# Performance work log

Measured on AMD Instinct MI355X. Metric: run time of the kernel, lower is better.

## Reference

```python
import jax, jax.numpy as jnp
import numpy as np

N_NODES = 10000
N_EDGES = 320000
D = 128
H = 4
C = 128
L = 2
NEG_SLOPE = 0.2
LN_EPS = 1e-5


def setup_inputs() -> dict:
    key = jax.random.key(0)
    ks = jax.random.split(key, 8)
    x = jax.random.normal(ks[0], (N_NODES, D), dtype=jnp.float32)
    edge_index = jax.random.randint(ks[1], (2, N_EDGES), 0, N_NODES, dtype=jnp.int64)
    # weights scaled ~Glorot to keep attention logits in a sane range
    Wl = jax.random.normal(ks[2], (L, D, H * C), dtype=jnp.float32) * 0.1
    Wr = jax.random.normal(ks[3], (L, D, H * C), dtype=jnp.float32) * 0.1
    att = jax.random.normal(ks[4], (L, H, C), dtype=jnp.float32) * 0.1
    return {
        "x": x,
        "edge_index": edge_index,
        "Wl": Wl,
        "bl": jnp.zeros((L, H * C), jnp.float32),
        "Wr": Wr,
        "br": jnp.zeros((L, H * C), jnp.float32),
        "att": att,
        "bias": jnp.zeros((L, D), jnp.float32),
        "ln_g": jnp.ones((L, D), jnp.float32),
        "ln_b": jnp.zeros((L, D), jnp.float32),
    }


def _gatv2_layer(x, src, dst, Wl, bl, Wr, br, att, b):
    """GATv2Conv (concat=False -> head mean), messages src->dst, softmax over dst."""
    n = x.shape[0]
    xl = (x @ Wl + bl).reshape(n, H, C)  # source transform
    xr = (x @ Wr + br).reshape(n, H, C)  # target transform
    s = jax.nn.leaky_relu(xl[src] + xr[dst], NEG_SLOPE)  # [E, H, C]
    e = jnp.einsum("ehc,hc->eh", s, att)  # attention logits [E, H]
    m = jax.ops.segment_max(e, dst, num_segments=n)  # stable softmax per dst segment
    ex = jnp.exp(e - m[dst])
    denom = jax.ops.segment_sum(ex, dst, num_segments=n)
    alpha = ex / denom[dst]  # [E, H]
    out = jax.ops.segment_sum(alpha[:, :, None] * xl[src], dst, num_segments=n)  # [N, H, C]
    return out.mean(axis=1) + b  # concat=False -> mean over heads, then bias


def _layer_norm(h, g, b):
    mu = h.mean(-1, keepdims=True)
    var = ((h - mu) ** 2).mean(-1, keepdims=True)
    return (h - mu) * jax.lax.rsqrt(var + LN_EPS) * g + b


def reference(x, edge_index, Wl, bl, Wr, br, att, bias, ln_g, ln_b):
    n = x.shape[0]
    loop = jnp.arange(n, dtype=edge_index.dtype)
    src = jnp.concatenate([edge_index[0], loop])  # add self-loops (PyG default)
    dst = jnp.concatenate([edge_index[1], loop])
    for i in range(L):
        h = _gatv2_layer(x, src, dst, Wl[i], bl[i], Wr[i], br[i], att[i], bias[i])
        x = h + x  # residual
        x = jax.nn.relu(_layer_norm(x, ln_g[i], ln_b[i]))
    return x
```

## Files before the change

kernel.cpp:

```cpp
#include <hip/hip_runtime.h>
#include <math.h>

#define N_NODES 10000
#define N_EDGES 320000
#define E_TOT   (N_EDGES + N_NODES)
#define NEG 0.2f
#define CAP 96

typedef short bf16x8 __attribute__((ext_vector_type(8)));
typedef float f32x4 __attribute__((ext_vector_type(4)));
typedef float f32x2 __attribute__((ext_vector_type(2)));

static __device__ __forceinline__ float4 ld4g(const float* p) { return *(const float4*)p; }

static __device__ __forceinline__ uint4 ldg4(const unsigned short* p, unsigned byteoff) {
    return *(const uint4*)((const char*)p + byteoff);
}

static __device__ __forceinline__ unsigned short f2b(float f) {
    unsigned u;
    __builtin_memcpy(&u, &f, 4);
    unsigned r = (u + 0x7fffu + ((u >> 16) & 1u)) >> 16;
    return (unsigned short)r;
}
static __device__ __forceinline__ f32x2 unpk(unsigned d) {
    f32x2 r;
    r.x = __uint_as_float(d << 16);
    r.y = __uint_as_float(d & 0xffff0000u);
    return r;
}

template <int CTRL>
static __device__ __forceinline__ float dpp_add_step(float x) {
    int y = __builtin_amdgcn_update_dpp(0, __float_as_int(x), CTRL, 0xf, 0xf, true);
    return x + __int_as_float(y);
}
static __device__ __forceinline__ float row_sum16(float x) {
    x = dpp_add_step<0x121>(x);
    x = dpp_add_step<0x122>(x);
    x = dpp_add_step<0x124>(x);
    x = dpp_add_step<0x128>(x);
    return x;
}

__global__ __launch_bounds__(256) void prep_fused_kernel(
    const float* __restrict__ x,
    const float* __restrict__ Wl, const float* __restrict__ Wr,
    unsigned short* __restrict__ xb, unsigned short* __restrict__ WT) {
    int tid = threadIdx.x, bid = blockIdx.x;
    __shared__ float tbuf[32][33];

    int l = bid >> 7;
    int rest = bid & 127;
    int ky = rest >> 5, nx = rest & 31;
    int n0 = nx * 32, k0 = ky * 32;
    const float* S = ((n0 < 512) ? Wl : Wr) + (size_t)l * 65536;
    int nn0 = n0 & 511;
    int tx = tid & 31, ty = tid >> 5;
#pragma unroll
    for (int it = 0; it < 4; ++it) {
        int k = k0 + ty + it * 8;
        tbuf[ty + it * 8][tx] = S[(size_t)k * 512 + nn0 + tx];
    }
    __syncthreads();
    unsigned short* dstp = WT + (size_t)l * 1024 * 128;
#pragma unroll
    for (int it = 0; it < 4; ++it) {
        int n = n0 + ty + it * 8;
        int k = k0 + tx;
        dstp[(size_t)n * 128 + k] = f2b(tbuf[tx][ty + it * 8]);
    }
    for (int i = bid * 256 + tid; i < N_NODES * 32; i += 256 * 256) {
        float4 v = ld4g(x + 4 * i);
        ushort4 o = make_ushort4(f2b(v.x), f2b(v.y), f2b(v.z), f2b(v.w));
        *(ushort4*)(xb + 4 * i) = o;
    }
}

__global__ void fill_bucket_kernel(const int* __restrict__ ei,
                                   int* __restrict__ deg, int* __restrict__ csr_src) {
    int i = blockIdx.x * blockDim.x + threadIdx.x;
    if (i >= E_TOT) return;
    bool is64 = ((ei[1] | ei[3] | ei[5] | ei[7]) == 0);
    int src, dst;
    if (i < N_EDGES) {
        if (is64) { const long long* e = (const long long*)ei; src = (int)e[i]; dst = (int)e[N_EDGES + i]; }
        else { src = ei[i]; dst = ei[N_EDGES + i]; }
    } else {
        src = dst = i - N_EDGES;
    }
    int pos = atomicAdd(&deg[dst], 1);
    if (pos < CAP) csr_src[dst * CAP + pos] = src;
}

__global__ __launch_bounds__(256) void gemm_mfma_kernel(const unsigned short* __restrict__ A,
                                                        const unsigned short* __restrict__ Bt,
                                                        const float* __restrict__ bl,
                                                        const float* __restrict__ br,
                                                        unsigned short* __restrict__ Y) {
    __shared__ unsigned short As[128][72];
    __shared__ unsigned short Bs[128][72];
    int tid = threadIdx.x;
    int wave = tid >> 6, lane = tid & 63;
    int wm = wave >> 1, wn = wave & 1;
    int l15 = lane & 15, quad = lane >> 4;
    int row0 = blockIdx.y * 128, col0 = blockIdx.x * 128;
    const float* bias = (col0 < 512) ? (bl + col0) : (br + col0 - 512);

    f32x4 acc[4][4];
#pragma unroll
    for (int mi = 0; mi < 4; ++mi)
#pragma unroll
        for (int ni = 0; ni < 4; ++ni)
#pragma unroll
            for (int r = 0; r < 4; ++r) acc[mi][ni][r] = 0.f;

#pragma unroll
    for (int kc = 0; kc < 2; ++kc) {
#pragma unroll
        for (int it = 0; it < 4; ++it) {
            int e = tid + it * 256;
            int r = e >> 3, s = e & 7;
            int gr = row0 + r;
            bf16x8 v = (bf16x8)(short)0;
            if (gr < N_NODES) v = *(const bf16x8*)(A + (size_t)gr * 128 + kc * 64 + s * 8);
            *(bf16x8*)&As[r][s * 8] = v;
            bf16x8 w = *(const bf16x8*)(Bt + (size_t)(col0 + r) * 128 + kc * 64 + s * 8);
            *(bf16x8*)&Bs[r][s * 8] = w;
        }
        __syncthreads();
#pragma unroll
        for (int kq = 0; kq < 2; ++kq) {
            bf16x8 af[4], bfr[4];
#pragma unroll
            for (int mi = 0; mi < 4; ++mi)
                af[mi] = *(const bf16x8*)&As[wm * 64 + mi * 16 + l15][kq * 32 + quad * 8];
#pragma unroll
            for (int ni = 0; ni < 4; ++ni)
                bfr[ni] = *(const bf16x8*)&Bs[wn * 64 + ni * 16 + l15][kq * 32 + quad * 8];
#pragma unroll
            for (int mi = 0; mi < 4; ++mi)
#pragma unroll
                for (int ni = 0; ni < 4; ++ni)
                    acc[mi][ni] = __builtin_amdgcn_mfma_f32_16x16x32_bf16(af[mi], bfr[ni], acc[mi][ni], 0, 0, 0);
        }
        __syncthreads();
    }

    float bv[4];
#pragma unroll
    for (int ni = 0; ni < 4; ++ni) bv[ni] = bias[wn * 64 + ni * 16 + l15];

#pragma unroll
    for (int mi = 0; mi < 4; ++mi) {
#pragma unroll
        for (int r = 0; r < 4; ++r) {
            int grow = row0 + wm * 64 + mi * 16 + quad * 4 + r;
            if (grow >= N_NODES) continue;
#pragma unroll
            for (int ni = 0; ni < 4; ++ni) {
                int gcol = col0 + wn * 64 + ni * 16 + l15;
                Y[(size_t)grow * 1024 + gcol] = f2b(acc[mi][ni][r] + bv[ni]);
            }
        }
    }
}

__global__ __launch_bounds__(256) void attn_kernel(
    const unsigned short* __restrict__ xlr,
    const float* __restrict__ x_in, const int* __restrict__ deg,
    const int* __restrict__ csr_src, const float* __restrict__ att,
    const float* __restrict__ bias, const float* __restrict__ ln_g,
    const float* __restrict__ ln_b, float* __restrict__ x_out,
    unsigned short* __restrict__ xb_out) {
    int wave = (blockIdx.x * blockDim.x + threadIdx.x) >> 6;
    int lane = threadIdx.x & 63;
    if (wave >= N_NODES) return;
    int dst = wave;
    int g = lane & 15;
    int off = 8 * lane;
    unsigned boff = (unsigned)off << 1;

    f32x2 xr2[4], at2[4];
    {
        uint4 u = ldg4(xlr, ((unsigned)dst << 11) + 1024u + boff);
        xr2[0] = unpk(u.x); xr2[1] = unpk(u.y); xr2[2] = unpk(u.z); xr2[3] = unpk(u.w);
        float4 a = ld4g(att + off);
        float4 b = ld4g(att + off + 4);
        at2[0].x = a.x; at2[0].y = a.y; at2[1].x = a.z; at2[1].y = a.w;
        at2[2].x = b.x; at2[2].y = b.y; at2[3].x = b.z; at2[3].y = b.w;
    }
    const f32x2 neg2 = {NEG, NEG};

    float d = 0.f;
    f32x2 acc2[4] = {{0.f, 0.f}, {0.f, 0.f}, {0.f, 0.f}, {0.f, 0.f}};

    int len = deg[dst];
    if (len > CAP) len = CAP;
    int beg = dst * CAP;
    int end = beg + len;
    int nfull = len & ~3;
    int pend = beg + nfull;
    int p = beg;

    if (nfull) {
        int i0 = csr_src[p], i1 = csr_src[p + 1], i2 = csr_src[p + 2], i3 = csr_src[p + 3];
        uint4 u0 = ldg4(xlr, ((unsigned)i0 << 11) + boff);
        uint4 u1 = ldg4(xlr, ((unsigned)i1 << 11) + boff);
        uint4 u2 = ldg4(xlr, ((unsigned)i2 << 11) + boff);
        uint4 u3 = ldg4(xlr, ((unsigned)i3 << 11) + boff);
        if (p + 4 < pend) {
            i0 = csr_src[p + 4]; i1 = csr_src[p + 5]; i2 = csr_src[p + 6]; i3 = csr_src[p + 7];
        }
        while (true) {
            p += 4;
            bool more = p < pend;
            uint4 n0, n1, n2, n3;
            if (more) {
                n0 = ldg4(xlr, ((unsigned)i0 << 11) + boff);
                n1 = ldg4(xlr, ((unsigned)i1 << 11) + boff);
                n2 = ldg4(xlr, ((unsigned)i2 << 11) + boff);
                n3 = ldg4(xlr, ((unsigned)i3 << 11) + boff);
                if (p + 4 < pend) {
                    i0 = csr_src[p + 4]; i1 = csr_src[p + 5];
                    i2 = csr_src[p + 6]; i3 = csr_src[p + 7];
                }
            }
            f32x2 F0[4], F1[4], F2[4], F3[4];
            {
                const unsigned* w0 = (const unsigned*)&u0;
                const unsigned* w1 = (const unsigned*)&u1;
                const unsigned* w2 = (const unsigned*)&u2;
                const unsigned* w3 = (const unsigned*)&u3;
#pragma unroll
                for (int q = 0; q < 4; ++q) {
                    F0[q] = unpk(w0[q]); F1[q] = unpk(w1[q]);
                    F2[q] = unpk(w2[q]); F3[q] = unpk(w3[q]);
                }
            }
            f32x2 q0 = {0.f, 0.f}, q1 = {0.f, 0.f}, q2 = {0.f, 0.f}, q3 = {0.f, 0.f};
#pragma unroll
            for (int q = 0; q < 4; ++q) {
                f32x2 s;
                s = F0[q] + xr2[q]; s = __builtin_elementwise_max(s, s * neg2);
                q0 = __builtin_elementwise_fma(s, at2[q], q0);
                s = F1[q] + xr2[q]; s = __builtin_elementwise_max(s, s * neg2);
                q1 = __builtin_elementwise_fma(s, at2[q], q1);
                s = F2[q] + xr2[q]; s = __builtin_elementwise_max(s, s * neg2);
                q2 = __builtin_elementwise_fma(s, at2[q], q2);
                s = F3[q] + xr2[q]; s = __builtin_elementwise_max(s, s * neg2);
                q3 = __builtin_elementwise_fma(s, at2[q], q3);
            }
            float p0 = row_sum16(q0.x + q0.y);
            float p1 = row_sum16(q1.x + q1.y);
            float p2 = row_sum16(q2.x + q2.y);
            float p3 = row_sum16(q3.x + q3.y);
            float e0 = __expf(p0), e1 = __expf(p1), e2 = __expf(p2), e3 = __expf(p3);
            d += (e0 + e1) + (e2 + e3);
            f32x2 W0 = {e0, e0}, W1 = {e1, e1}, W2 = {e2, e2}, W3 = {e3, e3};
#pragma unroll
            for (int q = 0; q < 4; ++q) {
                f32x2 t = __builtin_elementwise_fma(F0[q], W0, acc2[q]);
                t = __builtin_elementwise_fma(F1[q], W1, t);
                t = __builtin_elementwise_fma(F2[q], W2, t);
                acc2[q] = __builtin_elementwise_fma(F3[q], W3, t);
            }
            if (!more) break;
            u0 = n0; u1 = n1; u2 = n2; u3 = n3;
        }
    }
    for (; p < end; ++p) {
        int s0 = csr_src[p];
        uint4 u0 = ldg4(xlr, ((unsigned)s0 << 11) + boff);
        const unsigned* w0 = (const unsigned*)&u0;
        f32x2 F0[4];
#pragma unroll
        for (int q = 0; q < 4; ++q) F0[q] = unpk(w0[q]);
        f32x2 q0 = {0.f, 0.f};
#pragma unroll
        for (int q = 0; q < 4; ++q) {
            f32x2 s = F0[q] + xr2[q];
            s = __builtin_elementwise_max(s, s * neg2);
            q0 = __builtin_elementwise_fma(s, at2[q], q0);
        }
        float p0 = row_sum16(q0.x + q0.y);
        float e0 = __expf(p0);
        d += e0;
        f32x2 W0 = {e0, e0};
#pragma unroll
        for (int q = 0; q < 4; ++q)
            acc2[q] = __builtin_elementwise_fma(F0[q], W0, acc2[q]);
    }

    float inv = 1.f / d;
    float t[8];
#pragma unroll
    for (int q = 0; q < 4; ++q) {
        t[2 * q] = acc2[q].x * inv;
        t[2 * q + 1] = acc2[q].y * inv;
    }
#pragma unroll
    for (int j = 0; j < 8; ++j) {
        t[j] += __shfl_xor(t[j], 16, 64);
        t[j] += __shfl_xor(t[j], 32, 64);
    }
    float4 bi0 = ld4g(bias + 8 * g), bi1 = ld4g(bias + 8 * g + 4);
    float4 xi0 = ld4g(x_in + (size_t)dst * 128 + 8 * g);
    float4 xi1 = ld4g(x_in + (size_t)dst * 128 + 8 * g + 4);
    float hc[8];
    hc[0] = t[0] * 0.25f + bi0.x + xi0.x;
    hc[1] = t[1] * 0.25f + bi0.y + xi0.y;
    hc[2] = t[2] * 0.25f + bi0.z + xi0.z;
    hc[3] = t[3] * 0.25f + bi0.w + xi0.w;
    hc[4] = t[4] * 0.25f + bi1.x + xi1.x;
    hc[5] = t[5] * 0.25f + bi1.y + xi1.y;
    hc[6] = t[6] * 0.25f + bi1.z + xi1.z;
    hc[7] = t[7] * 0.25f + bi1.w + xi1.w;

    float sm = 0.f, sq = 0.f;
#pragma unroll
    for (int j = 0; j < 8; ++j) { sm += hc[j]; sq = fmaf(hc[j], hc[j], sq); }
    sm = row_sum16(sm);
    sq = row_sum16(sq);
    float mu = sm * (1.f / 128.f);
    float var = sq * (1.f / 128.f) - mu * mu;
    float rs = rsqrtf(var + 1e-5f);
    float4 g0 = ld4g(ln_g + 8 * g), g1 = ld4g(ln_g + 8 * g + 4);
    float4 b0 = ld4g(ln_b + 8 * g), b1 = ld4g(ln_b + 8 * g + 4);
    float y[8];
    y[0] = fmaxf((hc[0] - mu) * rs * g0.x + b0.x, 0.f);
    y[1] = fmaxf((hc[1] - mu) * rs * g0.y + b0.y, 0.f);
    y[2] = fmaxf((hc[2] - mu) * rs * g0.z + b0.z, 0.f);
    y[3] = fmaxf((hc[3] - mu) * rs * g0.w + b0.w, 0.f);
    y[4] = fmaxf((hc[4] - mu) * rs * g1.x + b1.x, 0.f);
    y[5] = fmaxf((hc[5] - mu) * rs * g1.y + b1.y, 0.f);
    y[6] = fmaxf((hc[6] - mu) * rs * g1.z + b1.z, 0.f);
    y[7] = fmaxf((hc[7] - mu) * rs * g1.w + b1.w, 0.f);

    if (lane < 16) {
        float4 o0 = make_float4(y[0], y[1], y[2], y[3]);
        float4 o1 = make_float4(y[4], y[5], y[6], y[7]);
        *(float4*)(x_out + (size_t)dst * 128 + 8 * g) = o0;
        *(float4*)(x_out + (size_t)dst * 128 + 8 * g + 4) = o1;
        if (xb_out) {
            ushort4 c0 = make_ushort4(f2b(y[0]), f2b(y[1]), f2b(y[2]), f2b(y[3]));
            ushort4 c1 = make_ushort4(f2b(y[4]), f2b(y[5]), f2b(y[6]), f2b(y[7]));
            *(ushort4*)(xb_out + (size_t)dst * 128 + 8 * g) = c0;
            *(ushort4*)(xb_out + (size_t)dst * 128 + 8 * g + 4) = c1;
        }
    }
}

extern "C" void kernel_launch(void* const* d_in, const int* in_sizes, int n_in,
                              void* d_out, int out_size, void* d_ws, size_t ws_size,
                              hipStream_t stream) {
    const float* x    = (const float*)d_in[0];
    const int*   ei   = (const int*)d_in[1];
    const float* Wl   = (const float*)d_in[2];
    const float* bl   = (const float*)d_in[3];
    const float* Wr   = (const float*)d_in[4];
    const float* br   = (const float*)d_in[5];
    const float* att  = (const float*)d_in[6];
    const float* bias = (const float*)d_in[7];
    const float* lng  = (const float*)d_in[8];
    const float* lnb  = (const float*)d_in[9];
    float* out = (float*)d_out;

    char* ws = (char*)d_ws;
    unsigned short* xlr = (unsigned short*)ws; ws += (size_t)N_NODES * 1024 * 2;
    float* xbuf  = (float*)ws;          ws += (size_t)N_NODES * 128 * 4;
    unsigned short* xb = (unsigned short*)ws; ws += (size_t)N_NODES * 128 * 2;
    unsigned short* WT = (unsigned short*)ws; ws += (size_t)2 * 1024 * 128 * 2;
    int* deg     = (int*)ws;            ws += (size_t)N_NODES * 4;
    int* csr_src = (int*)ws;            ws += (size_t)N_NODES * CAP * 4;

    hipMemsetAsync(deg, 0, N_NODES * sizeof(int), stream);
    prep_fused_kernel<<<256, 256, 0, stream>>>(x, Wl, Wr, xb, WT);
    fill_bucket_kernel<<<(E_TOT + 255) / 256, 256, 0, stream>>>(ei, deg, csr_src);

    for (int l = 0; l < 2; ++l) {
        const float* xin = (l == 0) ? x : xbuf;
        float* xout = (l == 0) ? xbuf : out;
        unsigned short* xbo = (l == 0) ? xb : (unsigned short*)nullptr;
        gemm_mfma_kernel<<<dim3(8, 79), 256, 0, stream>>>(xb, WT + (size_t)l * 1024 * 128,
                                                          bl + (size_t)l * 512,
                                                          br + (size_t)l * 512, xlr);
        attn_kernel<<<(N_NODES * 64 + 255) / 256, 256, 0, stream>>>(
            xlr, xin, deg, csr_src,
            att + (size_t)l * 512, bias + (size_t)l * 128,
            lng + (size_t)l * 128, lnb + (size_t)l * 128, xout, xbo);
    }
}
```

Baseline: 210.6 us.

## Fuse degree reset and edge bucketing into prep/GEMM, deepen gather prefetch

The separate memset and fill_bucket launches are removed. The deg reset moves into the prep kernel and edge bucketing is appended to the first-layer GEMM kernel as a grid-stride loop, which saves two launches and lets the bucketing atomics overlap with GEMM blocks. The attention kernel's neighbor gather now prefetches two groups of four source rows ahead instead of one, to hide more gather latency. The cost is higher register pressure in attn_kernel, and GEMM blocks now also carry the atomic scatter work.

Result: slower. 217.2 us (+3.1%).

```diff
diff --git a/kernel.cpp b/kernel.cpp
--- a/kernel.cpp
+++ b/kernel.cpp
@@ -46,9 +46,12 @@
 __global__ __launch_bounds__(256) void prep_fused_kernel(
     const float* __restrict__ x,
     const float* __restrict__ Wl, const float* __restrict__ Wr,
-    unsigned short* __restrict__ xb, unsigned short* __restrict__ WT) {
+    unsigned short* __restrict__ xb, unsigned short* __restrict__ WT,
+    int* __restrict__ deg) {
     int tid = threadIdx.x, bid = blockIdx.x;
     __shared__ float tbuf[32][33];
+
+    for (int i = bid * 256 + tid; i < N_NODES; i += 256 * 256) deg[i] = 0;
 
     int l = bid >> 7;
     int rest = bid & 127;
@@ -77,27 +80,15 @@
     }
 }
 
-__global__ void fill_bucket_kernel(const int* __restrict__ ei,
-                                   int* __restrict__ deg, int* __restrict__ csr_src) {
-    int i = blockIdx.x * blockDim.x + threadIdx.x;
-    if (i >= E_TOT) return;
-    bool is64 = ((ei[1] | ei[3] | ei[5] | ei[7]) == 0);
-    int src, dst;
-    if (i < N_EDGES) {
-        if (is64) { const long long* e = (const long long*)ei; src = (int)e[i]; dst = (int)e[N_EDGES + i]; }
-        else { src = ei[i]; dst = ei[N_EDGES + i]; }
-    } else {
-        src = dst = i - N_EDGES;
-    }
-    int pos = atomicAdd(&deg[dst], 1);
-    if (pos < CAP) csr_src[dst * CAP + pos] = src;
-}
-
+template <int DO_FILL>
 __global__ __launch_bounds__(256) void gemm_mfma_kernel(const unsigned short* __restrict__ A,
                                                         const unsigned short* __restrict__ Bt,
                                                         const float* __restrict__ bl,
                                                         const float* __restrict__ br,
-                                                        unsigned short* __restrict__ Y) {
+                                                        unsigned short* __restrict__ Y,
+                                                        const int* __restrict__ ei,
+                                                        int* __restrict__ deg,
+                                                        int* __restrict__ csr_src) {
     __shared__ unsigned short As[128][72];
     __shared__ unsigned short Bs[128][72];
     int tid = threadIdx.x;
@@ -162,6 +153,23 @@
                 int gcol = col0 + wn * 64 + ni * 16 + l15;
                 Y[(size_t)grow * 1024 + gcol] = f2b(acc[mi][ni][r] + bv[ni]);
             }
+        }
+    }
+
+    if (DO_FILL) {
+        bool is64 = ((ei[1] | ei[3] | ei[5] | ei[7]) == 0);
+        int nthreads = gridDim.x * gridDim.y * 256;
+        int gid = (blockIdx.y * gridDim.x + blockIdx.x) * 256 + tid;
+        for (int i = gid; i < E_TOT; i += nthreads) {
+            int src, dst;
+            if (i < N_EDGES) {
+                if (is64) { const long long* e = (const long long*)ei; src = (int)e[i]; dst = (int)e[N_EDGES + i]; }
+                else { src = ei[i]; dst = ei[N_EDGES + i]; }
+            } else {
+                src = dst = i - N_EDGES;
+            }
+            int pos = atomicAdd(&deg[dst], 1);
+            if (pos < CAP) csr_src[dst * CAP + pos] = src;
         }
     }
 }
@@ -204,34 +212,44 @@
     int p = beg;
 
     if (nfull) {
-        int i0 = csr_src[p], i1 = csr_src[p + 1], i2 = csr_src[p + 2], i3 = csr_src[p + 3];
-        uint4 u0 = ldg4(xlr, ((unsigned)i0 << 11) + boff);
-        uint4 u1 = ldg4(xlr, ((unsigned)i1 << 11) + boff);
-        uint4 u2 = ldg4(xlr, ((unsigned)i2 << 11) + boff);
-        uint4 u3 = ldg4(xlr, ((unsigned)i3 << 11) + boff);
+        int j0 = csr_src[p], j1 = csr_src[p + 1], j2 = csr_src[p + 2], j3 = csr_src[p + 3];
+        uint4 a0 = ldg4(xlr, ((unsigned)j0 << 11) + boff);
+        uint4 a1 = ldg4(xlr, ((unsigned)j1 << 11) + boff);
+        uint4 a2 = ldg4(xlr, ((unsigned)j2 << 11) + boff);
+        uint4 a3 = ldg4(xlr, ((unsigned)j3 << 11) + boff);
+        uint4 b0, b1, b2, b3;
+        int i0 = 0, i1 = 0, i2 = 0, i3 = 0;
         if (p + 4 < pend) {
-            i0 = csr_src[p + 4]; i1 = csr_src[p + 5]; i2 = csr_src[p + 6]; i3 = csr_src[p + 7];
+            j0 = csr_src[p + 4]; j1 = csr_src[p + 5]; j2 = csr_src[p + 6]; j3 = csr_src[p + 7];
+            b0 = ldg4(xlr, ((unsigned)j0 << 11) + boff);
+            b1 = ldg4(xlr, ((unsigned)j1 << 11) + boff);
+            b2 = ldg4(xlr, ((unsigned)j2 << 11) + boff);
+            b3 = ldg4(xlr, ((unsigned)j3 << 11) + boff);
+        }
+        if (p + 8 < pend) {
+            i0 = csr_src[p + 8]; i1 = csr_src[p + 9]; i2 = csr_src[p + 10]; i3 = csr_src[p + 11];
         }
         while (true) {
             p += 4;
-            bool more = p < pend;
-            uint4 n0, n1, n2, n3;
-            if (more) {
-                n0 = ldg4(xlr, ((unsigned)i0 << 11) + boff);
-                n1 = ldg4(xlr, ((unsigned)i1 << 11) + boff);
-                n2 = ldg4(xlr, ((unsigned)i2 << 11) + boff);
-                n3 = ldg4(xlr, ((unsigned)i3 << 11) + boff);
-                if (p + 4 < pend) {
-                    i0 = csr_src[p + 4]; i1 = csr_src[p + 5];
-                    i2 = csr_src[p + 6]; i3 = csr_src[p + 7];
+            bool more1 = p < pend;
+            bool more2 = p + 4 < pend;
+            uint4 c0, c1, c2, c3;
+            if (more2) {
+                c0 = ldg4(xlr, ((unsigned)i0 << 11) + boff);
+                c1 = ldg4(xlr, ((unsigned)i1 << 11) + boff);
+                c2 = ldg4(xlr, ((unsigned)i2 << 11) + boff);
+                c3 = ldg4(xlr, ((unsigned)i3 << 11) + boff);
+                if (p + 8 < pend) {
+                    i0 = csr_src[p + 8]; i1 = csr_src[p + 9];
+                    i2 = csr_src[p + 10]; i3 = csr_src[p + 11];
                 }
             }
             f32x2 F0[4], F1[4], F2[4], F3[4];
             {
-                const unsigned* w0 = (const unsigned*)&u0;
-                const unsigned* w1 = (const unsigned*)&u1;
-                const unsigned* w2 = (const unsigned*)&u2;
-                const unsigned* w3 = (const unsigned*)&u3;
+                const unsigned* w0 = (const unsigned*)&a0;
+                const unsigned* w1 = (const unsigned*)&a1;
+                const unsigned* w2 = (const unsigned*)&a2;
+                const unsigned* w3 = (const unsigned*)&a3;
 #pragma unroll
                 for (int q = 0; q < 4; ++q) {
                     F0[q] = unpk(w0[q]); F1[q] = unpk(w1[q]);
@@ -265,8 +283,9 @@
                 t = __builtin_elementwise_fma(F2[q], W2, t);
                 acc2[q] = __builtin_elementwise_fma(F3[q], W3, t);
             }
-            if (!more) break;
-            u0 = n0; u1 = n1; u2 = n2; u3 = n3;
+            if (!more1) break;
+            a0 = b0; a1 = b1; a2 = b2; a3 = b3;
+            if (more2) { b0 = c0; b1 = c1; b2 = c2; b3 = c3; }
         }
     }
     for (; p < end; ++p) {
@@ -374,17 +393,18 @@
     int* deg     = (int*)ws;            ws += (size_t)N_NODES * 4;
     int* csr_src = (int*)ws;            ws += (size_t)N_NODES * CAP * 4;
 
-    hipMemsetAsync(deg, 0, N_NODES * sizeof(int), stream);
-    prep_fused_kernel<<<256, 256, 0, stream>>>(x, Wl, Wr, xb, WT);
-    fill_bucket_kernel<<<(E_TOT + 255) / 256, 256, 0, stream>>>(ei, deg, csr_src);
+    prep_fused_kernel<<<256, 256, 0, stream>>>(x, Wl, Wr, xb, WT, deg);
 
     for (int l = 0; l < 2; ++l) {
         const float* xin = (l == 0) ? x : xbuf;
         float* xout = (l == 0) ? xbuf : out;
         unsigned short* xbo = (l == 0) ? xb : (unsigned short*)nullptr;
-        gemm_mfma_kernel<<<dim3(8, 79), 256, 0, stream>>>(xb, WT + (size_t)l * 1024 * 128,
-                                                          bl + (size_t)l * 512,
-                                                          br + (size_t)l * 512, xlr);
+        if (l == 0)
+            gemm_mfma_kernel<1><<<dim3(8, 79), 256, 0, stream>>>(
+                xb, WT, bl, br, xlr, ei, deg, csr_src);
+        else
+            gemm_mfma_kernel<0><<<dim3(8, 79), 256, 0, stream>>>(
+                xb, WT + (size_t)1024 * 128, bl + 512, br + 512, xlr, ei, deg, csr_src);
         attn_kernel<<<(N_NODES * 64 + 255) / 256, 256, 0, stream>>>(
             xlr, xin, deg, csr_src,
             att + (size_t)l * 512, bias + (size_t)l * 128,
```
